# Kernel optimization log

Measured on AMD Instinct MI355X. Metric: run time of the kernel, lower is better.

## Reference

```python
import jax, jax.numpy as jnp
import numpy as np


def sparsemax_last(z):
    """Sparsemax over the last axis (Martins & Astudillo 2016)."""
    dims = z.shape[-1]
    z_sorted = jnp.sort(z, axis=-1)[..., ::-1]          # descending
    z_cumsum = jnp.cumsum(z_sorted, axis=-1)
    k = jnp.arange(1, dims + 1, dtype=z.dtype)
    support = 1.0 + k * z_sorted > z_cumsum              # [..., dims] bool
    k_z = jnp.sum(support.astype(jnp.int32), axis=-1)    # support size >= 1 for finite z
    tau_sum = jnp.take_along_axis(z_cumsum, (k_z - 1)[..., None], axis=-1)[..., 0]
    tau = (tau_sum - 1.0) / k_z.astype(z.dtype)
    return jnp.maximum(z - tau[..., None], 0.0)


def _bin_codes_1hot(depth, dtype):
    n_leaf = 2 ** depth
    indices = np.arange(n_leaf)
    offsets = 2 ** np.arange(depth)
    codes = (indices[None, :] // offsets[:, None]) % 2   # [depth, 2^depth]
    onehot = np.stack([codes, 1 - codes], axis=-1)       # [depth, 2^depth, 2]
    return jnp.asarray(onehot, dtype=dtype)


def setup_inputs() -> dict:
    key = jax.random.key(0)
    ks = jax.random.split(key, 5)
    B, I, N, D, U = 1024, 256, 512, 6, 16
    return {
        "x": jax.random.normal(ks[0], (B, I), dtype=jnp.float32),
        "feature_selection_logits": jax.random.normal(ks[1], (I, N, D), dtype=jnp.float32),
        "feature_thresholds": jax.random.normal(ks[2], (N, D), dtype=jnp.float32),
        "log_temperatures": jax.random.normal(ks[3], (N, D), dtype=jnp.float32) * 0.1,
        "response": jax.random.normal(ks[4], (N, U, 2 ** D), dtype=jnp.float32),
    }


def reference(x, feature_selection_logits, feature_thresholds, log_temperatures, response):
    depth = feature_thresholds.shape[1]
    # feature selection via sparsemax over depth axis (axis=-1, as in source)
    feature_selectors = sparsemax_last(feature_selection_logits)          # [I,N,D]
    feature_values = jnp.einsum('bi,ind->bnd', x, feature_selectors)      # [B,N,D]
    # temperature-scaled threshold logits
    tl = (feature_values - feature_thresholds) * jnp.exp(-log_temperatures)
    tl = jnp.stack([-tl, tl], axis=-1)                                    # [B,N,D,2]
    bins = jnp.clip(0.5 * tl + 0.5, 0.0, 1.0)                             # sparsemoid
    onehot = _bin_codes_1hot(depth, bins.dtype)                           # [D,2^D,2]
    bin_matches = jnp.einsum('btds,dcs->btdc', bins, onehot)              # [B,N,D,2^D]
    response_weights = jnp.prod(bin_matches, axis=-2)                     # [B,N,2^D]
    out = jnp.einsum('bnd,ncd->bnc', response_weights, response)          # [B,N,U]
    return jnp.sum(out, axis=1)                                           # [B,U]
```

## Files before the change

kernel.cpp:

```cpp
#include <hip/hip_runtime.h>
#include <hip/hip_bf16.h>

#define B_SZ 1024
#define I_SZ 256
#define N_SZ 512
#define D_SZ 6
#define U_SZ 16
#define C_SZ 64
#define NSPLIT 64

typedef __bf16 bf16_t;
typedef bf16_t bf16x8 __attribute__((ext_vector_type(8)));
typedef float  f32x4  __attribute__((ext_vector_type(4)));


__global__ __launch_bounds__(256) void prep_pack(
    const float* __restrict__ fsl, const float* __restrict__ x,
    const float* __restrict__ resp, const float* __restrict__ th,
    const float* __restrict__ lt,
    bf16_t* __restrict__ selF, bf16_t* __restrict__ xbF,
    bf16_t* __restrict__ respF, float2* __restrict__ sb,
    float* __restrict__ out) {
  __shared__ float smem[4160];
  const int bid = blockIdx.x, t = threadIdx.x;

  if (bid < 512) {
    float (*sT)[17] = (float(*)[17])smem;
    const int nb = bid & 31, ib = bid >> 5;
    const int i_loc = t >> 4, n_loc = t & 15;
    const int n0 = nb * 16, i0 = ib * 16;

    const float* z = fsl + ((size_t)(i0 + i_loc) * N_SZ + (n0 + n_loc)) * D_SZ;
    float v[D_SZ], s[D_SZ];
#pragma unroll
    for (int d = 0; d < D_SZ; ++d) { v[d] = z[d]; s[d] = v[d]; }
#define CSWAP(a, b) { float hi = fmaxf(s[a], s[b]); float lo = fminf(s[a], s[b]); s[a] = hi; s[b] = lo; }
#pragma unroll
    for (int r = 0; r < 3; ++r) {
      CSWAP(0, 1) CSWAP(2, 3) CSWAP(4, 5)
      CSWAP(1, 2) CSWAP(3, 4)
    }
#undef CSWAP
    float cs[D_SZ];
    cs[0] = s[0];
#pragma unroll
    for (int j = 1; j < D_SZ; ++j) cs[j] = cs[j - 1] + s[j];
    int kz = 0;
#pragma unroll
    for (int j = 0; j < D_SZ; ++j)
      kz += (1.0f + (float)(j + 1) * s[j] > cs[j]) ? 1 : 0;
    const float tau = (cs[kz - 1] - 1.0f) / (float)kz;
#pragma unroll
    for (int d = 0; d < D_SZ; ++d)
      sT[n_loc * 6 + d][i_loc] = fmaxf(v[d] - tau, 0.0f);
    __syncthreads();

    if (t < 192) {
      const int r = t >> 1, h = t & 1;
      const int g  = 6 * nb + (r >> 4), lm = r & 15;
      const int kk = ib >> 1, q = (ib & 1) * 2 + h;
      bf16x8 o;
#pragma unroll
      for (int jj = 0; jj < 8; ++jj) o[jj] = (bf16_t)sT[r][h * 8 + jj];
      *(bf16x8*)(selF + ((size_t)(g * 8 + kk) * 64 + q * 16 + lm) * 8) = o;
    }
  } else if (bid < 576) {
    float (*xs)[257] = (float(*)[257])smem;
    const int gb = bid - 512;
#pragma unroll
    for (int c = 0; c < 4; ++c) {
      const int e = c * 256 + t;
      const int row = e >> 6, col = (e & 63) * 4;
      const float4 v = *(const float4*)(x + (size_t)(gb * 16 + row) * I_SZ + col);
      xs[row][col] = v.x; xs[row][col + 1] = v.y;
      xs[row][col + 2] = v.z; xs[row][col + 3] = v.w;
    }
    __syncthreads();
#pragma unroll
    for (int h = 0; h < 2; ++h) {
      const int fid = h * 256 + t;
      const int kk = fid >> 6, lane = fid & 63;
      const int lm = lane & 15, q = lane >> 4;
      bf16x8 o;
#pragma unroll
      for (int jj = 0; jj < 8; ++jj) o[jj] = (bf16_t)xs[lm][kk * 32 + q * 8 + jj];
      *(bf16x8*)(xbF + ((size_t)(gb * 8 + kk) * 64 + lane) * 8) = o;
    }
  } else if (bid < 704) {
    float (*rs)[16][65] = (float(*)[16][65])smem;
    const int n0 = (bid - 576) * 4;
#pragma unroll
    for (int c = 0; c < 4; ++c) {
      const int e = c * 256 + t;
      const int n_loc = e >> 8, idx = (e & 255) * 4;
      const int u = idx >> 6, cc = idx & 63;
      const float4 v = *(const float4*)(resp + (size_t)(n0 + n_loc) * 1024 + idx);
      rs[n_loc][u][cc] = v.x; rs[n_loc][u][cc + 1] = v.y;
      rs[n_loc][u][cc + 2] = v.z; rs[n_loc][u][cc + 3] = v.w;
    }
    __syncthreads();
#pragma unroll
    for (int h = 0; h < 2; ++h) {
      const int fid = h * 256 + t;
      const int n_loc = fid >> 7, chunk = (fid >> 6) & 1, lane = fid & 63;
      const int lm = lane & 15, q = lane >> 4;
      bf16x8 o;
#pragma unroll
      for (int jj = 0; jj < 8; ++jj)
        o[jj] = (bf16_t)rs[n_loc][lm][chunk * 32 + q * 8 + jj];
      *(bf16x8*)(respF + ((size_t)((n0 + n_loc) * 2 + chunk) * 64 + lane) * 8) = o;
    }
  } else if (bid < 720) {
    const int idx = ((bid - 704) * 256 + t) * 4;
    *(float4*)(out + idx) = make_float4(0.f, 0.f, 0.f, 0.f);
  } else {
    const int i = (bid - 720) * 256 + t;
    const float sc = __expf(-lt[i]);
    sb[i] = make_float2(sc, -th[i] * sc);
  }
}

__global__ __launch_bounds__(256, 4) void fused_k(
    const bf16_t* __restrict__ selF,
    const bf16_t* __restrict__ xbF,
    const float2* __restrict__ sb,
    const bf16_t* __restrict__ respF,
    float* __restrict__ out) {
  __shared__ float fv[48][68];
  const int t = threadIdx.x;
  const int lane = t & 63, wave = t >> 6;
  const int lm = lane & 15, q = lane >> 4;
  const int btile = blockIdx.x & 15, ns = blockIdx.x >> 4;

  bf16x8 rpre[8];
  {
    f32x4 acc[3];
#pragma unroll
    for (int kg = 0; kg < 3; ++kg) acc[kg] = (f32x4){0.f, 0.f, 0.f, 0.f};
    const bf16_t* aF = selF + ((size_t)(ns * 3) * 8 * 64 + lane) * 8;
    const bf16_t* bF = xbF + ((size_t)(btile * 4 + wave) * 8 * 64 + lane) * 8;
#pragma unroll
    for (int kk = 0; kk < 8; ++kk) {
      const bf16x8 bv = *(const bf16x8*)(bF + (size_t)kk * 64 * 8);
#pragma unroll
      for (int kg = 0; kg < 3; ++kg) {
        const bf16x8 a = *(const bf16x8*)(aF + (size_t)(kg * 8 + kk) * 64 * 8);
        acc[kg] = __builtin_amdgcn_mfma_f32_16x16x32_bf16(a, bv, acc[kg], 0, 0, 0);
      }
    }

    const bf16_t* rF0 = respF + ((size_t)(ns * 8) * 2 * 64 + lane) * 8;
#pragma unroll
    for (int p = 0; p < 8; ++p)
      rpre[p] = *(const bf16x8*)(rF0 + (size_t)p * 64 * 8);

#pragma unroll
    for (int kg = 0; kg < 3; ++kg)
#pragma unroll
      for (int r = 0; r < 4; ++r) {
        const float2 sv = sb[ns * 48 + kg * 16 + q * 4 + r];
        fv[kg * 16 + q * 4 + r][wave * 16 + lm] = fmaf(acc[kg][r], sv.x, sv.y);
      }
  }
  __syncthreads();

  f32x4 acc = (f32x4){0.f, 0.f, 0.f, 0.f};
  const int bloc = wave * 16 + lm;

#pragma unroll
  for (int j = 0; j < 8; ++j) {
    const int n = ns * 8 + j;
    bf16x8 bv0, bv1;
    if (j < 4) {
      bv0 = rpre[j * 2]; bv1 = rpre[j * 2 + 1];
    } else {
      const bf16_t* rF = respF + ((size_t)n * 2 * 64 + lane) * 8;
      bv0 = *(const bf16x8*)(rF);
      bv1 = *(const bf16x8*)(rF + 64 * 8);
    }

    float b0v[D_SZ], b1v[D_SZ];
#pragma unroll
    for (int d = 0; d < D_SZ; ++d) {
      const float tl = fv[j * 6 + d][bloc];
      b1v[d] = fminf(fmaxf(0.5f * tl + 0.5f, 0.0f), 1.0f);
      b0v[d] = fminf(fmaxf(0.5f - 0.5f * tl, 0.0f), 1.0f);
    }
    float p2[2], p4[4], p8[8];
    p2[0] = b1v[0]; p2[1] = b0v[0];
#pragma unroll
    for (int i = 0; i < 4; ++i) p4[i] = p2[i & 1] * ((i & 2) ? b0v[1] : b1v[1]);
#pragma unroll
    for (int i = 0; i < 8; ++i) p8[i] = p4[i & 3] * ((i & 4) ? b0v[2] : b1v[2]);
    const float f3 = (q & 1) ? b0v[3] : b1v[3];
    const float f4 = (q & 2) ? b0v[4] : b1v[4];
    const float fq = f3 * f4;
    const float g0 = fq * b1v[5];
    const float g1 = fq * b0v[5];

    bf16x8 a0, a1;
#pragma unroll
    for (int jj = 0; jj < 8; ++jj) {
      a0[jj] = (bf16_t)(p8[jj] * g0);
      a1[jj] = (bf16_t)(p8[jj] * g1);
    }
    acc = __builtin_amdgcn_mfma_f32_16x16x32_bf16(a0, bv0, acc, 0, 0, 0);
    acc = __builtin_amdgcn_mfma_f32_16x16x32_bf16(a1, bv1, acc, 0, 0, 0);
  }

  float* obase = out + (size_t)(btile * 64 + wave * 16) * U_SZ;
#pragma unroll
  for (int r = 0; r < 4; ++r)
    atomicAdd(&obase[(q * 4 + r) * U_SZ + lm], acc[r]);
}

extern "C" void kernel_launch(void* const* d_in, const int* in_sizes, int n_in,
                              void* d_out, int out_size, void* d_ws, size_t ws_size,
                              hipStream_t stream) {
  const float* x    = (const float*)d_in[0];
  const float* fsl  = (const float*)d_in[1];
  const float* th   = (const float*)d_in[2];
  const float* lt   = (const float*)d_in[3];
  const float* resp = (const float*)d_in[4];
  float* out = (float*)d_out;

  char* w = (char*)d_ws;
  bf16_t* selF  = (bf16_t*)(w);
  bf16_t* xbF   = (bf16_t*)(w + 1572864);
  bf16_t* respF = (bf16_t*)(w + 2097152);
  float2* sb    = (float2*)(w + 3145728);

  prep_pack<<<732, 256, 0, stream>>>(fsl, x, resp, th, lt,
                                     selF, xbF, respF, sb, out);

  fused_k<<<16 * NSPLIT, 256, 0, stream>>>(selF, xbF, sb, respF, out);
}
```

Baseline: 77.20 us.

## Fuse sparsemax and packing prep into the main kernel, drop workspace round-trip

Removes the separate prep_pack kernel. Each block now computes sparsemax for its own 8-tree slice into shared memory, converts x and response tiles from fp32 to bf16 in registers, and computes the temperature scale/bias locally. The output is zeroed with a memset instead. This avoids one kernel launch and the global workspace write/read. In exchange, sparsemax work is repeated across the 16 batch tiles, and fp32 inputs are read redundantly with more global traffic per block.

Result: slower. 94.49 us (+22.4%).

```diff
diff --git a/kernel.cpp b/kernel.cpp
--- a/kernel.cpp
+++ b/kernel.cpp
@@ -6,7 +6,6 @@
 #define N_SZ 512
 #define D_SZ 6
 #define U_SZ 16
-#define C_SZ 64
 #define NSPLIT 64
 
 typedef __bf16 bf16_t;
@@ -14,154 +13,99 @@
 typedef float  f32x4  __attribute__((ext_vector_type(4)));
 
 
-__global__ __launch_bounds__(256) void prep_pack(
+__global__ __launch_bounds__(256, 4) void odst_fused(
     const float* __restrict__ fsl, const float* __restrict__ x,
     const float* __restrict__ resp, const float* __restrict__ th,
-    const float* __restrict__ lt,
-    bf16_t* __restrict__ selF, bf16_t* __restrict__ xbF,
-    bf16_t* __restrict__ respF, float2* __restrict__ sb,
-    float* __restrict__ out) {
-  __shared__ float smem[4160];
-  const int bid = blockIdx.x, t = threadIdx.x;
+    const float* __restrict__ lt, float* __restrict__ out) {
+  __shared__ char smem[25728];
+  bf16_t (*sT)[264] = (bf16_t(*)[264])smem;
+  float2* sbs = (float2*)(smem + 25344);
+  float (*fv)[68] = (float(*)[68])smem;
 
-  if (bid < 512) {
-    float (*sT)[17] = (float(*)[17])smem;
-    const int nb = bid & 31, ib = bid >> 5;
-    const int i_loc = t >> 4, n_loc = t & 15;
-    const int n0 = nb * 16, i0 = ib * 16;
-
-    const float* z = fsl + ((size_t)(i0 + i_loc) * N_SZ + (n0 + n_loc)) * D_SZ;
-    float v[D_SZ], s[D_SZ];
-#pragma unroll
-    for (int d = 0; d < D_SZ; ++d) { v[d] = z[d]; s[d] = v[d]; }
-#define CSWAP(a, b) { float hi = fmaxf(s[a], s[b]); float lo = fminf(s[a], s[b]); s[a] = hi; s[b] = lo; }
-#pragma unroll
-    for (int r = 0; r < 3; ++r) {
-      CSWAP(0, 1) CSWAP(2, 3) CSWAP(4, 5)
-      CSWAP(1, 2) CSWAP(3, 4)
-    }
-#undef CSWAP
-    float cs[D_SZ];
-    cs[0] = s[0];
-#pragma unroll
-    for (int j = 1; j < D_SZ; ++j) cs[j] = cs[j - 1] + s[j];
-    int kz = 0;
-#pragma unroll
-    for (int j = 0; j < D_SZ; ++j)
-      kz += (1.0f + (float)(j + 1) * s[j] > cs[j]) ? 1 : 0;
-    const float tau = (cs[kz - 1] - 1.0f) / (float)kz;
-#pragma unroll
-    for (int d = 0; d < D_SZ; ++d)
-      sT[n_loc * 6 + d][i_loc] = fmaxf(v[d] - tau, 0.0f);
-    __syncthreads();
-
-    if (t < 192) {
-      const int r = t >> 1, h = t & 1;
-      const int g  = 6 * nb + (r >> 4), lm = r & 15;
-      const int kk = ib >> 1, q = (ib & 1) * 2 + h;
-      bf16x8 o;
-#pragma unroll
-      for (int jj = 0; jj < 8; ++jj) o[jj] = (bf16_t)sT[r][h * 8 + jj];
-      *(bf16x8*)(selF + ((size_t)(g * 8 + kk) * 64 + q * 16 + lm) * 8) = o;
-    }
-  } else if (bid < 576) {
-    float (*xs)[257] = (float(*)[257])smem;
-    const int gb = bid - 512;
-#pragma unroll
-    for (int c = 0; c < 4; ++c) {
-      const int e = c * 256 + t;
-      const int row = e >> 6, col = (e & 63) * 4;
-      const float4 v = *(const float4*)(x + (size_t)(gb * 16 + row) * I_SZ + col);
-      xs[row][col] = v.x; xs[row][col + 1] = v.y;
-      xs[row][col + 2] = v.z; xs[row][col + 3] = v.w;
-    }
-    __syncthreads();
-#pragma unroll
-    for (int h = 0; h < 2; ++h) {
-      const int fid = h * 256 + t;
-      const int kk = fid >> 6, lane = fid & 63;
-      const int lm = lane & 15, q = lane >> 4;
-      bf16x8 o;
-#pragma unroll
-      for (int jj = 0; jj < 8; ++jj) o[jj] = (bf16_t)xs[lm][kk * 32 + q * 8 + jj];
-      *(bf16x8*)(xbF + ((size_t)(gb * 8 + kk) * 64 + lane) * 8) = o;
-    }
-  } else if (bid < 704) {
-    float (*rs)[16][65] = (float(*)[16][65])smem;
-    const int n0 = (bid - 576) * 4;
-#pragma unroll
-    for (int c = 0; c < 4; ++c) {
-      const int e = c * 256 + t;
-      const int n_loc = e >> 8, idx = (e & 255) * 4;
-      const int u = idx >> 6, cc = idx & 63;
-      const float4 v = *(const float4*)(resp + (size_t)(n0 + n_loc) * 1024 + idx);
-      rs[n_loc][u][cc] = v.x; rs[n_loc][u][cc + 1] = v.y;
-      rs[n_loc][u][cc + 2] = v.z; rs[n_loc][u][cc + 3] = v.w;
-    }
-    __syncthreads();
-#pragma unroll
-    for (int h = 0; h < 2; ++h) {
-      const int fid = h * 256 + t;
-      const int n_loc = fid >> 7, chunk = (fid >> 6) & 1, lane = fid & 63;
-      const int lm = lane & 15, q = lane >> 4;
-      bf16x8 o;
-#pragma unroll
-      for (int jj = 0; jj < 8; ++jj)
-        o[jj] = (bf16_t)rs[n_loc][lm][chunk * 32 + q * 8 + jj];
-      *(bf16x8*)(respF + ((size_t)((n0 + n_loc) * 2 + chunk) * 64 + lane) * 8) = o;
-    }
-  } else if (bid < 720) {
-    const int idx = ((bid - 704) * 256 + t) * 4;
-    *(float4*)(out + idx) = make_float4(0.f, 0.f, 0.f, 0.f);
-  } else {
-    const int i = (bid - 720) * 256 + t;
-    const float sc = __expf(-lt[i]);
-    sb[i] = make_float2(sc, -th[i] * sc);
-  }
-}
-
-__global__ __launch_bounds__(256, 4) void fused_k(
-    const bf16_t* __restrict__ selF,
-    const bf16_t* __restrict__ xbF,
-    const float2* __restrict__ sb,
-    const bf16_t* __restrict__ respF,
-    float* __restrict__ out) {
-  __shared__ float fv[48][68];
   const int t = threadIdx.x;
   const int lane = t & 63, wave = t >> 6;
   const int lm = lane & 15, q = lane >> 4;
   const int btile = blockIdx.x & 15, ns = blockIdx.x >> 4;
 
-  bf16x8 rpre[8];
+  if (t < 48) {
+    const int kp = ns * 48 + t;
+    const float sc = __expf(-lt[kp]);
+    sbs[t] = make_float2(sc, -th[kp] * sc);
+  }
+
   {
-    f32x4 acc[3];
+    float buf[48];
+    const float* zb = fsl + ((size_t)t * N_SZ + ns * 8) * D_SZ;
 #pragma unroll
-    for (int kg = 0; kg < 3; ++kg) acc[kg] = (f32x4){0.f, 0.f, 0.f, 0.f};
-    const bf16_t* aF = selF + ((size_t)(ns * 3) * 8 * 64 + lane) * 8;
-    const bf16_t* bF = xbF + ((size_t)(btile * 4 + wave) * 8 * 64 + lane) * 8;
+    for (int c = 0; c < 12; ++c)
+      *(float4*)&buf[c * 4] = *(const float4*)(zb + c * 4);
+
+#pragma unroll
+    for (int nl = 0; nl < 8; ++nl) {
+      float v[D_SZ], s[D_SZ];
+#pragma unroll
+      for (int d = 0; d < D_SZ; ++d) { v[d] = buf[nl * 6 + d]; s[d] = v[d]; }
+#define CSWAP(a, b) { float hi = fmaxf(s[a], s[b]); float lo = fminf(s[a], s[b]); s[a] = hi; s[b] = lo; }
+#pragma unroll
+      for (int r = 0; r < 3; ++r) {
+        CSWAP(0, 1) CSWAP(2, 3) CSWAP(4, 5)
+        CSWAP(1, 2) CSWAP(3, 4)
+      }
+#undef CSWAP
+      float cs[D_SZ];
+      cs[0] = s[0];
+#pragma unroll
+      for (int j = 1; j < D_SZ; ++j) cs[j] = cs[j - 1] + s[j];
+      int kz = 0;
+#pragma unroll
+      for (int j = 0; j < D_SZ; ++j)
+        kz += (1.0f + (float)(j + 1) * s[j] > cs[j]) ? 1 : 0;
+      const float tau = (cs[kz - 1] - 1.0f) / (float)kz;
+#pragma unroll
+      for (int d = 0; d < D_SZ; ++d)
+        sT[nl * 6 + d][t] = (bf16_t)fmaxf(v[d] - tau, 0.0f);
+    }
+  }
+  __syncthreads();
+
+  f32x4 acc3[3];
+#pragma unroll
+  for (int kg = 0; kg < 3; ++kg) acc3[kg] = (f32x4){0.f, 0.f, 0.f, 0.f};
+  {
+    const float* xw = x + (size_t)(btile * 64 + wave * 16 + lm) * I_SZ + q * 8;
 #pragma unroll
     for (int kk = 0; kk < 8; ++kk) {
-      const bf16x8 bv = *(const bf16x8*)(bF + (size_t)kk * 64 * 8);
+      float xf[8];
+      *(float4*)&xf[0] = *(const float4*)(xw + kk * 32);
+      *(float4*)&xf[4] = *(const float4*)(xw + kk * 32 + 4);
+      bf16x8 bv;
+#pragma unroll
+      for (int jj = 0; jj < 8; ++jj) bv[jj] = (bf16_t)xf[jj];
 #pragma unroll
       for (int kg = 0; kg < 3; ++kg) {
-        const bf16x8 a = *(const bf16x8*)(aF + (size_t)(kg * 8 + kk) * 64 * 8);
-        acc[kg] = __builtin_amdgcn_mfma_f32_16x16x32_bf16(a, bv, acc[kg], 0, 0, 0);
+        const bf16x8 a = *(const bf16x8*)&sT[kg * 16 + lm][kk * 32 + q * 8];
+        acc3[kg] = __builtin_amdgcn_mfma_f32_16x16x32_bf16(a, bv, acc3[kg], 0, 0, 0);
       }
     }
+  }
 
-    const bf16_t* rF0 = respF + ((size_t)(ns * 8) * 2 * 64 + lane) * 8;
+  float rp[32];
+  const float* rbase = resp + (size_t)(ns * 8) * 1024 + lm * 64 + q * 8;
 #pragma unroll
-    for (int p = 0; p < 8; ++p)
-      rpre[p] = *(const bf16x8*)(rF0 + (size_t)p * 64 * 8);
+  for (int jc = 0; jc < 4; ++jc) {
+    const float* p = rbase + (jc >> 1) * 1024 + (jc & 1) * 32;
+    *(float4*)&rp[jc * 8]     = *(const float4*)(p);
+    *(float4*)&rp[jc * 8 + 4] = *(const float4*)(p + 4);
+  }
 
+  __syncthreads();
 #pragma unroll
-    for (int kg = 0; kg < 3; ++kg)
+  for (int kg = 0; kg < 3; ++kg)
 #pragma unroll
-      for (int r = 0; r < 4; ++r) {
-        const float2 sv = sb[ns * 48 + kg * 16 + q * 4 + r];
-        fv[kg * 16 + q * 4 + r][wave * 16 + lm] = fmaf(acc[kg][r], sv.x, sv.y);
-      }
-  }
+    for (int r = 0; r < 4; ++r) {
+      const float2 sv = sbs[kg * 16 + q * 4 + r];
+      fv[kg * 16 + q * 4 + r][wave * 16 + lm] = fmaf(acc3[kg][r], sv.x, sv.y);
+    }
   __syncthreads();
 
   f32x4 acc = (f32x4){0.f, 0.f, 0.f, 0.f};
@@ -169,14 +113,25 @@
 
 #pragma unroll
   for (int j = 0; j < 8; ++j) {
-    const int n = ns * 8 + j;
     bf16x8 bv0, bv1;
-    if (j < 4) {
-      bv0 = rpre[j * 2]; bv1 = rpre[j * 2 + 1];
+    if (j < 2) {
+#pragma unroll
+      for (int jj = 0; jj < 8; ++jj) {
+        bv0[jj] = (bf16_t)rp[(j * 2) * 8 + jj];
+        bv1[jj] = (bf16_t)rp[(j * 2 + 1) * 8 + jj];
+      }
     } else {
-      const bf16_t* rF = respF + ((size_t)n * 2 * 64 + lane) * 8;
-      bv0 = *(const bf16x8*)(rF);
-      bv1 = *(const bf16x8*)(rF + 64 * 8);
+      const float* p = rbase + (size_t)j * 1024;
+      float rf[16];
+      *(float4*)&rf[0]  = *(const float4*)(p);
+      *(float4*)&rf[4]  = *(const float4*)(p + 4);
+      *(float4*)&rf[8]  = *(const float4*)(p + 32);
+      *(float4*)&rf[12] = *(const float4*)(p + 36);
+#pragma unroll
+      for (int jj = 0; jj < 8; ++jj) {
+        bv0[jj] = (bf16_t)rf[jj];
+        bv1[jj] = (bf16_t)rf[8 + jj];
+      }
     }
 
     float b0v[D_SZ], b1v[D_SZ];
@@ -224,14 +179,7 @@
   const float* resp = (const float*)d_in[4];
   float* out = (float*)d_out;
 
-  char* w = (char*)d_ws;
-  bf16_t* selF  = (bf16_t*)(w);
-  bf16_t* xbF   = (bf16_t*)(w + 1572864);
-  bf16_t* respF = (bf16_t*)(w + 2097152);
-  float2* sb    = (float2*)(w + 3145728);
+  hipMemsetAsync(out, 0, (size_t)B_SZ * U_SZ * sizeof(float), stream);
 
-  prep_pack<<<732, 256, 0, stream>>>(fsl, x, resp, th, lt,
-                                     selF, xbF, respF, sb, out);
-
-  fused_k<<<16 * NSPLIT, 256, 0, stream>>>(selF, xbF, sb, respF, out);
+  odst_fused<<<16 * NSPLIT, 256, 0, stream>>>(fsl, x, resp, th, lt, out);
 }
```
